# Performance work log

Measured on AMD Instinct MI355X. Metric: run time of the kernel, lower is better.

## Reference

```python
import jax, jax.numpy as jnp
import numpy as np

# Vanilla tanh-RNN (num_layers=1, batch_first) followed by tanh + dropout(eval: identity) + linear.

def setup_inputs() -> dict:
    key = jax.random.key(0)
    ks = jax.random.split(key, 7)
    B, T, I, H, C = 16384, 64, 64, 100, 40
    s_ih = 1.0 / np.sqrt(H)
    return {
        "x": jax.random.normal(ks[0], (B, T * I), dtype=jnp.float32),
        "W_ih": jax.random.normal(ks[1], (H, I), dtype=jnp.float32) * s_ih,
        "W_hh": jax.random.normal(ks[2], (H, H), dtype=jnp.float32) * s_ih,
        "b_ih": jax.random.normal(ks[3], (H,), dtype=jnp.float32) * s_ih,
        "b_hh": jax.random.normal(ks[4], (H,), dtype=jnp.float32) * s_ih,
        "fc_W": jax.random.normal(ks[5], (C, H), dtype=jnp.float32) * 0.1,
        "fc_b": jax.random.normal(ks[6], (C,), dtype=jnp.float32) * 0.1,
    }


def reference(x, W_ih, W_hh, b_ih, b_hh, fc_W, fc_b):
    B = x.shape[0]
    x = x.reshape(B, 64, 64)  # [B, T, I]
    # Precompute input projections for all steps in one GEMM: [B, T, H]
    xp = jnp.einsum("bti,hi->bth", x, W_ih) + b_ih + b_hh
    h0 = jnp.zeros((B, W_hh.shape[0]), dtype=x.dtype)

    def step(h, xp_t):  # h: [B, H], xp_t: [B, H]
        h_new = jnp.tanh(xp_t + h @ W_hh.T)
        return h_new, None

    h_last, _ = jax.lax.scan(step, h0, jnp.swapaxes(xp, 0, 1))  # scan over T
    out = jnp.tanh(h_last)  # tanh on last-step output
    # dropout(p=0.2) in eval mode = identity
    return out @ fc_W.T + fc_b  # [B, 40]
```

## Files before the change

### kernel.cpp

```cpp
#include <hip/hip_runtime.h>


typedef _Float16 half8 __attribute__((ext_vector_type(8)));
typedef _Float16 half4_t __attribute__((ext_vector_type(4)));
typedef float float4_t __attribute__((ext_vector_type(4)));

#define LDSROW 132

__device__ __forceinline__ float tanh_fast(float x) {
  float e = __builtin_amdgcn_exp2f(x * 2.8853900817779268f);
  return 1.0f - 2.0f * __builtin_amdgcn_rcpf(e + 1.0f);
}

__global__ __launch_bounds__(256, 1) void rnn_fused(
    const float* __restrict__ x, const float* __restrict__ W_ih,
    const float* __restrict__ W_hh, const float* __restrict__ b_ih,
    const float* __restrict__ b_hh, const float* __restrict__ fc_W,
    const float* __restrict__ fc_b, float* __restrict__ out, int B)
{
  __shared__ _Float16 lds[4][16 * LDSROW];
  const int lane = threadIdx.x & 63;
  const int wave = threadIdx.x >> 6;
  const int g = lane >> 4;
  const int c = lane & 15;
  _Float16* h_lds = lds[wave];

  const int rowbase = (blockIdx.x * 4 + wave) * 16;
  if (rowbase >= B) return;

  {
    int* p = (int*)h_lds;
    #pragma unroll
    for (int i = 0; i < 17; ++i) {
      int idx = lane + i * 64;
      if (idx < 16 * LDSROW / 2) p[idx] = 0;
    }
  }

  half8 wih[2][7];
  half8 whh[4][7];
  float4_t biasv[7];
  #pragma unroll
  for (int nt = 0; nt < 7; ++nt) {
    int n = nt * 16 + c;
    bool nv = (n < 100);
    float bb = nv ? (b_ih[n] + b_hh[n]) : 0.0f;
    biasv[nt] = (float4_t){bb, bb, bb, bb};
    #pragma unroll
    for (int kb = 0; kb < 2; ++kb) {
      float4_t f0 = {0,0,0,0}, f1 = {0,0,0,0};
      if (nv) {
        const float* p = W_ih + n * 64 + kb * 32 + g * 8;
        f0 = *(const float4_t*)p;
        f1 = *(const float4_t*)(p + 4);
      }
      half8 h;
      #pragma unroll
      for (int j = 0; j < 4; ++j) { h[j] = (_Float16)f0[j]; h[4+j] = (_Float16)f1[j]; }
      wih[kb][nt] = h;
    }
    #pragma unroll
    for (int kb = 0; kb < 4; ++kb) {
      int k = kb * 32 + g * 8;
      float4_t f0 = {0,0,0,0}, f1 = {0,0,0,0};
      if (nv && k < 100) {
        const float* p = W_hh + n * 100 + k;
        f0 = *(const float4_t*)p;
        if (k <= 92) f1 = *(const float4_t*)(p + 4);
      }
      half8 h;
      #pragma unroll
      for (int j = 0; j < 4; ++j) { h[j] = (_Float16)f0[j]; h[4+j] = (_Float16)f1[j]; }
      whh[kb][nt] = h;
    }
  }

  const float* xrow = x + (size_t)(rowbase + c) * 4096;
  float4_t s0, s1, s2, s3;
  {
    const float* p = xrow + g * 8;
    s0 = *(const float4_t*)p;        s1 = *(const float4_t*)(p + 4);
    s2 = *(const float4_t*)(p + 32); s3 = *(const float4_t*)(p + 36);
  }

  float4_t acc[7];

  for (int t = 0; t < 64; ++t) {
    float4_t n0 = {0,0,0,0}, n1 = {0,0,0,0}, n2 = {0,0,0,0}, n3 = {0,0,0,0};
    if (t < 63) {
      const float* p = xrow + (t + 1) * 64 + g * 8;
      n0 = *(const float4_t*)p;        n1 = *(const float4_t*)(p + 4);
      n2 = *(const float4_t*)(p + 32); n3 = *(const float4_t*)(p + 36);
    }

    half8 xa0, xa1;
    #pragma unroll
    for (int j = 0; j < 4; ++j) {
      xa0[j]   = (_Float16)s0[j]; xa0[4+j] = (_Float16)s1[j];
      xa1[j]   = (_Float16)s2[j]; xa1[4+j] = (_Float16)s3[j];
    }

    #pragma unroll
    for (int nt = 0; nt < 7; ++nt) {
      acc[nt] = __builtin_amdgcn_mfma_f32_16x16x32_f16(xa0, wih[0][nt], biasv[nt], 0, 0, 0);
      acc[nt] = __builtin_amdgcn_mfma_f32_16x16x32_f16(xa1, wih[1][nt], acc[nt], 0, 0, 0);
    }

    #pragma unroll
    for (int kb = 0; kb < 4; ++kb) {
      half4_t lo = *(const half4_t*)&h_lds[c * LDSROW + kb * 32 + g * 8];
      half4_t hi = *(const half4_t*)&h_lds[c * LDSROW + kb * 32 + g * 8 + 4];
      half8 ha;
      #pragma unroll
      for (int j = 0; j < 4; ++j) { ha[j] = lo[j]; ha[4+j] = hi[j]; }
      #pragma unroll
      for (int nt = 0; nt < 7; ++nt)
        acc[nt] = __builtin_amdgcn_mfma_f32_16x16x32_f16(ha, whh[kb][nt], acc[nt], 0, 0, 0);
    }

    #pragma unroll
    for (int nt = 0; nt < 7; ++nt) {
      #pragma unroll
      for (int v = 0; v < 4; ++v) {
        float th = tanh_fast(acc[nt][v]);
        acc[nt][v] = th;
        if (nt < 6 || c < 4)
          h_lds[(g * 4 + v) * LDSROW + nt * 16 + c] = (_Float16)th;
      }
    }

    s0 = n0; s1 = n1; s2 = n2; s3 = n3;
  }

  #pragma unroll
  for (int nt = 0; nt < 7; ++nt) {
    #pragma unroll
    for (int v = 0; v < 4; ++v) {
      float th2 = tanh_fast(acc[nt][v]);
      if (nt < 6 || c < 4)
        h_lds[(g * 4 + v) * LDSROW + nt * 16 + c] = (_Float16)th2;
    }
  }

  half8 wfc[4][3];
  float4_t bfc[3];
  #pragma unroll
  for (int nt = 0; nt < 3; ++nt) {
    int n = nt * 16 + c;
    bool nv = (n < 40);
    float bb = nv ? fc_b[n] : 0.0f;
    bfc[nt] = (float4_t){bb, bb, bb, bb};
    #pragma unroll
    for (int kb = 0; kb < 4; ++kb) {
      int k = kb * 32 + g * 8;
      float4_t f0 = {0,0,0,0}, f1 = {0,0,0,0};
      if (nv && k < 100) {
        const float* p = fc_W + n * 100 + k;
        f0 = *(const float4_t*)p;
        if (k <= 92) f1 = *(const float4_t*)(p + 4);
      }
      half8 h;
      #pragma unroll
      for (int j = 0; j < 4; ++j) { h[j] = (_Float16)f0[j]; h[4+j] = (_Float16)f1[j]; }
      wfc[kb][nt] = h;
    }
  }

  float4_t oacc[3];
  #pragma unroll
  for (int kb = 0; kb < 4; ++kb) {
    half4_t lo = *(const half4_t*)&h_lds[c * LDSROW + kb * 32 + g * 8];
    half4_t hi = *(const half4_t*)&h_lds[c * LDSROW + kb * 32 + g * 8 + 4];
    half8 ha;
    #pragma unroll
    for (int j = 0; j < 4; ++j) { ha[j] = lo[j]; ha[4+j] = hi[j]; }
    #pragma unroll
    for (int nt = 0; nt < 3; ++nt)
      oacc[nt] = __builtin_amdgcn_mfma_f32_16x16x32_f16(
          ha, wfc[kb][nt], (kb == 0) ? bfc[nt] : oacc[nt], 0, 0, 0);
  }

  #pragma unroll
  for (int nt = 0; nt < 3; ++nt) {
    #pragma unroll
    for (int v = 0; v < 4; ++v) {
      int n = nt * 16 + c;
      if (n < 40) {
        int r = rowbase + g * 4 + v;
        out[(size_t)r * 40 + n] = oacc[nt][v];
      }
    }
  }
}

extern "C" void kernel_launch(void* const* d_in, const int* in_sizes, int n_in,
                              void* d_out, int out_size, void* d_ws, size_t ws_size,
                              hipStream_t stream) {
  const float* x    = (const float*)d_in[0];
  const float* W_ih = (const float*)d_in[1];
  const float* W_hh = (const float*)d_in[2];
  const float* b_ih = (const float*)d_in[3];
  const float* b_hh = (const float*)d_in[4];
  const float* fc_W = (const float*)d_in[5];
  const float* fc_b = (const float*)d_in[6];
  float* outp = (float*)d_out;

  int B = in_sizes[0] / 4096;
  int grid = (B + 63) / 64;
  rnn_fused<<<grid, 256, 0, stream>>>(x, W_ih, W_hh, b_ih, b_hh, fc_W, fc_b, outp, B);
}
```

Baseline: 73.72 us.

## Transpose MFMA operands so hidden state stays in registers, eliminating LDS round-trip

```diff
diff --git a/kernel.cpp b/kernel.cpp
--- a/kernel.cpp
+++ b/kernel.cpp
@@ -2,10 +2,7 @@
 
 
 typedef _Float16 half8 __attribute__((ext_vector_type(8)));
-typedef _Float16 half4_t __attribute__((ext_vector_type(4)));
 typedef float float4_t __attribute__((ext_vector_type(4)));
-
-#define LDSROW 132
 
 __device__ __forceinline__ float tanh_fast(float x) {
   float e = __builtin_amdgcn_exp2f(x * 2.8853900817779268f);
@@ -18,179 +15,178 @@
     const float* __restrict__ b_hh, const float* __restrict__ fc_W,
     const float* __restrict__ fc_b, float* __restrict__ out, int B)
 {
-  __shared__ _Float16 lds[4][16 * LDSROW];
   const int lane = threadIdx.x & 63;
   const int wave = threadIdx.x >> 6;
   const int g = lane >> 4;
   const int c = lane & 15;
-  _Float16* h_lds = lds[wave];
-
   const int rowbase = (blockIdx.x * 4 + wave) * 16;
-  if (rowbase >= B) return;
-
-  {
-    int* p = (int*)h_lds;
-    #pragma unroll
-    for (int i = 0; i < 17; ++i) {
-      int idx = lane + i * 64;
-      if (idx < 16 * LDSROW / 2) p[idx] = 0;
-    }
-  }
 
   half8 wih[2][7];
   half8 whh[4][7];
-  float4_t biasv[7];
+  float4_t bias[7];
+
   #pragma unroll
   for (int nt = 0; nt < 7; ++nt) {
-    int n = nt * 16 + c;
-    bool nv = (n < 100);
-    float bb = nv ? (b_ih[n] + b_hh[n]) : 0.0f;
-    biasv[nt] = (float4_t){bb, bb, bb, bb};
+    int nb = nt * 16 + 4 * g;
+    float4_t bi = {0.f, 0.f, 0.f, 0.f};
+    if (nb + 3 < 100) {
+      float4_t a = *(const float4_t*)(b_ih + nb);
+      float4_t b = *(const float4_t*)(b_hh + nb);
+      bi = a + b;
+    }
+    bias[nt] = bi;
+
+    int nrow = nt * 16 + c;
+    bool rv = (nrow < 100);
     #pragma unroll
     for (int kb = 0; kb < 2; ++kb) {
-      float4_t f0 = {0,0,0,0}, f1 = {0,0,0,0};
-      if (nv) {
-        const float* p = W_ih + n * 64 + kb * 32 + g * 8;
+      float4_t f0 = {0.f,0.f,0.f,0.f}, f1 = {0.f,0.f,0.f,0.f};
+      if (rv) {
+        const float* p = W_ih + nrow * 64 + kb * 32 + g * 8;
         f0 = *(const float4_t*)p;
         f1 = *(const float4_t*)(p + 4);
       }
       half8 h;
       #pragma unroll
-      for (int j = 0; j < 4; ++j) { h[j] = (_Float16)f0[j]; h[4+j] = (_Float16)f1[j]; }
+      for (int j = 0; j < 4; ++j) { h[j] = (_Float16)f0[j]; h[4 + j] = (_Float16)f1[j]; }
       wih[kb][nt] = h;
     }
     #pragma unroll
     for (int kb = 0; kb < 4; ++kb) {
-      int k = kb * 32 + g * 8;
-      float4_t f0 = {0,0,0,0}, f1 = {0,0,0,0};
-      if (nv && k < 100) {
-        const float* p = W_hh + n * 100 + k;
-        f0 = *(const float4_t*)p;
-        if (k <= 92) f1 = *(const float4_t*)(p + 4);
-      }
-      half8 h;
-      #pragma unroll
-      for (int j = 0; j < 4; ++j) { h[j] = (_Float16)f0[j]; h[4+j] = (_Float16)f1[j]; }
+      int clo = kb * 32 + 4 * g;
+      int chi = clo + 16;
+      float4_t f0 = {0.f,0.f,0.f,0.f}, f1 = {0.f,0.f,0.f,0.f};
+      if (rv && clo + 3 < 100) f0 = *(const float4_t*)(W_hh + nrow * 100 + clo);
+      if (rv && chi + 3 < 100) f1 = *(const float4_t*)(W_hh + nrow * 100 + chi);
+      half8 h;
+      #pragma unroll
+      for (int j = 0; j < 4; ++j) { h[j] = (_Float16)f0[j]; h[4 + j] = (_Float16)f1[j]; }
       whh[kb][nt] = h;
     }
   }
 
-  const float* xrow = x + (size_t)(rowbase + c) * 4096;
+  const float* xrow = x + (size_t)(rowbase + c) * 4096 + g * 8;
   float4_t s0, s1, s2, s3;
+  float4_t p0, p1, p2, p3;
   {
-    const float* p = xrow + g * 8;
+    const float* p = xrow;
     s0 = *(const float4_t*)p;        s1 = *(const float4_t*)(p + 4);
     s2 = *(const float4_t*)(p + 32); s3 = *(const float4_t*)(p + 36);
+    p += 64;
+    p0 = *(const float4_t*)p;        p1 = *(const float4_t*)(p + 4);
+    p2 = *(const float4_t*)(p + 32); p3 = *(const float4_t*)(p + 36);
   }
 
   float4_t acc[7];
+  half8 hfrag[4];
+  #pragma unroll
+  for (int kb = 0; kb < 4; ++kb) hfrag[kb] = (half8)(_Float16)0.0f;
 
   for (int t = 0; t < 64; ++t) {
-    float4_t n0 = {0,0,0,0}, n1 = {0,0,0,0}, n2 = {0,0,0,0}, n3 = {0,0,0,0};
-    if (t < 63) {
-      const float* p = xrow + (t + 1) * 64 + g * 8;
-      n0 = *(const float4_t*)p;        n1 = *(const float4_t*)(p + 4);
-      n2 = *(const float4_t*)(p + 32); n3 = *(const float4_t*)(p + 36);
-    }
-
-    half8 xa0, xa1;
+    float4_t q0 = {0.f,0.f,0.f,0.f}, q1 = q0, q2 = q0, q3 = q0;
+    if (t < 62) {
+      const float* p = xrow + (t + 2) * 64;
+      q0 = *(const float4_t*)p;        q1 = *(const float4_t*)(p + 4);
+      q2 = *(const float4_t*)(p + 32); q3 = *(const float4_t*)(p + 36);
+    }
+
+    half8 xb0, xb1;
     #pragma unroll
     for (int j = 0; j < 4; ++j) {
-      xa0[j]   = (_Float16)s0[j]; xa0[4+j] = (_Float16)s1[j];
-      xa1[j]   = (_Float16)s2[j]; xa1[4+j] = (_Float16)s3[j];
+      xb0[j] = (_Float16)s0[j]; xb0[4 + j] = (_Float16)s1[j];
+      xb1[j] = (_Float16)s2[j]; xb1[4 + j] = (_Float16)s3[j];
     }
 
     #pragma unroll
     for (int nt = 0; nt < 7; ++nt) {
-      acc[nt] = __builtin_amdgcn_mfma_f32_16x16x32_f16(xa0, wih[0][nt], biasv[nt], 0, 0, 0);
-      acc[nt] = __builtin_amdgcn_mfma_f32_16x16x32_f16(xa1, wih[1][nt], acc[nt], 0, 0, 0);
-    }
+      acc[nt] = __builtin_amdgcn_mfma_f32_16x16x32_f16(wih[0][nt], xb0, bias[nt], 0, 0, 0);
+      acc[nt] = __builtin_amdgcn_mfma_f32_16x16x32_f16(wih[1][nt], xb1, acc[nt], 0, 0, 0);
+    }
+    #pragma unroll
+    for (int kb = 0; kb < 4; ++kb)
+      #pragma unroll
+      for (int nt = 0; nt < 7; ++nt)
+        acc[nt] = __builtin_amdgcn_mfma_f32_16x16x32_f16(whh[kb][nt], hfrag[kb], acc[nt], 0, 0, 0);
+
+    #pragma unroll
+    for (int nt = 0; nt < 7; ++nt)
+      #pragma unroll
+      for (int v = 0; v < 4; ++v)
+        acc[nt][v] = tanh_fast(acc[nt][v]);
 
     #pragma unroll
     for (int kb = 0; kb < 4; ++kb) {
-      half4_t lo = *(const half4_t*)&h_lds[c * LDSROW + kb * 32 + g * 8];
-      half4_t hi = *(const half4_t*)&h_lds[c * LDSROW + kb * 32 + g * 8 + 4];
-      half8 ha;
-      #pragma unroll
-      for (int j = 0; j < 4; ++j) { ha[j] = lo[j]; ha[4+j] = hi[j]; }
-      #pragma unroll
-      for (int nt = 0; nt < 7; ++nt)
-        acc[nt] = __builtin_amdgcn_mfma_f32_16x16x32_f16(ha, whh[kb][nt], acc[nt], 0, 0, 0);
-    }
-
-    #pragma unroll
-    for (int nt = 0; nt < 7; ++nt) {
+      half8 h;
       #pragma unroll
       for (int v = 0; v < 4; ++v) {
-        float th = tanh_fast(acc[nt][v]);
-        acc[nt][v] = th;
-        if (nt < 6 || c < 4)
-          h_lds[(g * 4 + v) * LDSROW + nt * 16 + c] = (_Float16)th;
+        h[v] = (_Float16)acc[2 * kb][v];
+        h[4 + v] = (kb < 3) ? (_Float16)acc[2 * kb + 1][v] : (_Float16)0.0f;
       }
-    }
-
-    s0 = n0; s1 = n1; s2 = n2; s3 = n3;
-  }
-
-  #pragma unroll
-  for (int nt = 0; nt < 7; ++nt) {
+      hfrag[kb] = h;
+    }
+
+    s0 = p0; s1 = p1; s2 = p2; s3 = p3;
+    p0 = q0; p1 = q1; p2 = q2; p3 = q3;
+  }
+
+  #pragma unroll
+  for (int nt = 0; nt < 7; ++nt)
+    #pragma unroll
+    for (int v = 0; v < 4; ++v)
+      acc[nt][v] = tanh_fast(acc[nt][v]);
+  #pragma unroll
+  for (int kb = 0; kb < 4; ++kb) {
+    half8 h;
     #pragma unroll
     for (int v = 0; v < 4; ++v) {
-      float th2 = tanh_fast(acc[nt][v]);
-      if (nt < 6 || c < 4)
-        h_lds[(g * 4 + v) * LDSROW + nt * 16 + c] = (_Float16)th2;
-    }
+      h[v] = (_Float16)acc[2 * kb][v];
+      h[4 + v] = (kb < 3) ? (_Float16)acc[2 * kb + 1][v] : (_Float16)0.0f;
+    }
+    hfrag[kb] = h;
   }
 
   half8 wfc[4][3];
   float4_t bfc[3];
   #pragma unroll
   for (int nt = 0; nt < 3; ++nt) {
-    int n = nt * 16 + c;
-    bool nv = (n < 40);
-    float bb = nv ? fc_b[n] : 0.0f;
-    bfc[nt] = (float4_t){bb, bb, bb, bb};
+    int nb = nt * 16 + 4 * g;
+    float4_t bi = {0.f,0.f,0.f,0.f};
+    if (nb + 3 < 40) bi = *(const float4_t*)(fc_b + nb);
+    bfc[nt] = bi;
+
+    int nrow = nt * 16 + c;
+    bool rv = (nrow < 40);
     #pragma unroll
     for (int kb = 0; kb < 4; ++kb) {
-      int k = kb * 32 + g * 8;
-      float4_t f0 = {0,0,0,0}, f1 = {0,0,0,0};
-      if (nv && k < 100) {
-        const float* p = fc_W + n * 100 + k;
-        f0 = *(const float4_t*)p;
-        if (k <= 92) f1 = *(const float4_t*)(p + 4);
-      }
-      half8 h;
-      #pragma unroll
-      for (int j = 0; j < 4; ++j) { h[j] = (_Float16)f0[j]; h[4+j] = (_Float16)f1[j]; }
+      int clo = kb * 32 + 4 * g;
+      int chi = clo + 16;
+      float4_t f0 = {0.f,0.f,0.f,0.f}, f1 = {0.f,0.f,0.f,0.f};
+      if (rv && clo + 3 < 100) f0 = *(const float4_t*)(fc_W + nrow * 100 + clo);
+      if (rv && chi + 3 < 100) f1 = *(const float4_t*)(fc_W + nrow * 100 + chi);
+      half8 h;
+      #pragma unroll
+      for (int j = 0; j < 4; ++j) { h[j] = (_Float16)f0[j]; h[4 + j] = (_Float16)f1[j]; }
       wfc[kb][nt] = h;
     }
   }
 
   float4_t oacc[3];
   #pragma unroll
-  for (int kb = 0; kb < 4; ++kb) {
-    half4_t lo = *(const half4_t*)&h_lds[c * LDSROW + kb * 32 + g * 8];
-    half4_t hi = *(const half4_t*)&h_lds[c * LDSROW + kb * 32 + g * 8 + 4];
-    half8 ha;
-    #pragma unroll
-    for (int j = 0; j < 4; ++j) { ha[j] = lo[j]; ha[4+j] = hi[j]; }
+  for (int nt = 0; nt < 3; ++nt) oacc[nt] = bfc[nt];
+  #pragma unroll
+  for (int kb = 0; kb < 4; ++kb)
     #pragma unroll
     for (int nt = 0; nt < 3; ++nt)
-      oacc[nt] = __builtin_amdgcn_mfma_f32_16x16x32_f16(
-          ha, wfc[kb][nt], (kb == 0) ? bfc[nt] : oacc[nt], 0, 0, 0);
-  }
-
-  #pragma unroll
-  for (int nt = 0; nt < 3; ++nt) {
+      oacc[nt] = __builtin_amdgcn_mfma_f32_16x16x32_f16(wfc[kb][nt], hfrag[kb], oacc[nt], 0, 0, 0);
+
+  #pragma unroll
+  for (int nt = 0; nt < 3; ++nt)
     #pragma unroll
     for (int v = 0; v < 4; ++v) {
-      int n = nt * 16 + c;
-      if (n < 40) {
-        int r = rowbase + g * 4 + v;
-        out[(size_t)r * 40 + n] = oacc[nt][v];
-      }
-    }
-  }
+      int n = nt * 16 + 4 * g + v;
+      if (n < 40)
+        out[(size_t)(rowbase + c) * 40 + n] = oacc[nt][v];
+    }
 }
 
 extern "C" void kernel_launch(void* const* d_in, const int* in_sizes, int n_in,
```

After: 68.48 us. 7.1% less time.
